# Kernel tuning notes

Measured on AMD Instinct MI355X. Metric: run time of the kernel, lower is better.

Reference implementation:

```python
import jax, jax.numpy as jnp
import numpy as np

EPS = 1e-06


def setup_inputs() -> dict:
    key = jax.random.key(0)
    k1, k2 = jax.random.split(key)
    x = jax.random.normal(k1, (8, 128, 256, 256), dtype=jnp.float32)
    weights = jax.random.normal(k2, (128,), dtype=jnp.float32)
    return {"x": x, "weights": weights}


def reference(x, weights):
    # x: [b, q, h, w]; weights: [q]
    q = weights.shape[0]
    norm_const = jnp.float32(q)
    # use_cumsum=False path: softmax over features, scaled by norm_const
    wt = jax.nn.softmax(weights) * norm_const  # [q]
    # rank[b,i,h,w] = rank of x[b,i,h,w] when sorting dim 1 descending
    order = jnp.argsort(-x, axis=1)            # descending argsort
    rank = jnp.argsort(order, axis=1)          # inverse permutation -> ranks
    # gather per-rank weight and apply 1/sqrt(x^2 + eps)
    return wt[rank] * jax.lax.rsqrt(x * x + jnp.float32(EPS))
```

## Files before the change

kernel.cpp:

```cpp
#include <hip/hip_runtime.h>
#include <math.h>


#define Q    128
#define TCOL 64
#define HW   65536
#define EPSF 1e-6f

__device__ __forceinline__ void acc_ge(int& rk, float a, float b) {
    unsigned long long c, dead;
    asm("v_cmp_ge_f32 %0, %1, %2" : "=s"(c) : "v"(a), "v"(b));
    asm("v_addc_co_u32 %0, %1, %0, 0, %2" : "+v"(rk), "=s"(dead) : "s"(c));
}
__device__ __forceinline__ void acc_gt(int& rk, float a, float b) {
    unsigned long long c, dead;
    asm("v_cmp_gt_f32 %0, %1, %2" : "=s"(c) : "v"(a), "v"(b));
    asm("v_addc_co_u32 %0, %1, %0, 0, %2" : "+v"(rk), "=s"(dead) : "s"(c));
}
__device__ __forceinline__ void pair_upd(int& rkb, int& rka, float va, float vb) {
    unsigned long long c, d1, d2;
    asm("v_cmp_ge_f32 %0, %1, %2" : "=s"(c) : "v"(va), "v"(vb));
    asm("v_addc_co_u32 %0, %1, %0, 0, %2" : "+v"(rkb), "=s"(d1) : "s"(c));
    asm("v_subb_co_u32 %0, %1, %0, 0, %2" : "+v"(rka), "=s"(d2) : "s"(c));
}

__launch_bounds__(256, 4)
__global__ void rank_weight_kernel(const float* __restrict__ x,
                                   const float* __restrict__ weights,
                                   float* __restrict__ out) {
    __shared__ float lds_x[Q][TCOL];
    __shared__ float lds_wt[Q];

    const int tid = threadIdx.x;
    const int g   = blockIdx.x;
    const int b   = g >> 10;
    const int hw0 = (g & 1023) << 6;
    const float* xb = x   + (size_t)b * Q * HW + hw0;
    float*       ob = out + (size_t)b * Q * HW + hw0;

    for (int f = tid; f < Q * (TCOL / 4); f += 256) {
        const int r = f >> 4;
        const int p = f & 15;
        float4 val = *reinterpret_cast<const float4*>(xb + (size_t)r * HW + (p << 2));
        *reinterpret_cast<float4*>(&lds_x[r][p << 2]) = val;
    }

    if (tid < 64) {
        float w0 = weights[tid];
        float w1 = weights[tid + 64];
        float m = fmaxf(w0, w1);
        #pragma unroll
        for (int off = 32; off; off >>= 1) m = fmaxf(m, __shfl_xor(m, off, 64));
        float e0 = __expf(w0 - m), e1 = __expf(w1 - m);
        float s = e0 + e1;
        #pragma unroll
        for (int off = 32; off; off >>= 1) s += __shfl_xor(s, off, 64);
        float scale = 128.0f / s;
        lds_wt[tid]      = e0 * scale;
        lds_wt[tid + 64] = e1 * scale;
    }
    __syncthreads();

    const int wave = tid >> 6;
    const int c    = tid & 63;
    const int R0   = wave * 32;

    float v[32];
    int   rk[32];
    #pragma unroll
    for (int u = 0; u < 32; ++u) v[u] = lds_x[R0 + u][c];
    #pragma unroll
    for (int u = 0; u < 32; ++u) rk[u] = 31 - u;

    #pragma unroll
    for (int a = 0; a < 32; ++a) {
        #pragma unroll
        for (int bq = a + 1; bq < 32; ++bq) pair_upd(rk[bq], rk[a], v[a], v[bq]);
    }

    for (int j = 0; j < R0; j += 2) {
        float w0 = lds_x[j][c];
        float w1 = lds_x[j + 1][c];
        #pragma unroll
        for (int u = 0; u < 32; ++u) acc_ge(rk[u], w0, v[u]);
        #pragma unroll
        for (int u = 0; u < 32; ++u) acc_ge(rk[u], w1, v[u]);
    }
    for (int j = R0 + 32; j < Q; j += 2) {
        float w0 = lds_x[j][c];
        float w1 = lds_x[j + 1][c];
        #pragma unroll
        for (int u = 0; u < 32; ++u) acc_gt(rk[u], w0, v[u]);
        #pragma unroll
        for (int u = 0; u < 32; ++u) acc_gt(rk[u], w1, v[u]);
    }

    #pragma unroll
    for (int u = 0; u < 32; ++u) {
        float wt  = lds_wt[rk[u]];
        float val = v[u];
        ob[(size_t)(R0 + u) * HW + c] = wt * rsqrtf(val * val + EPSF);
    }
}

extern "C" void kernel_launch(void* const* d_in, const int* in_sizes, int n_in,
                              void* d_out, int out_size, void* d_ws, size_t ws_size,
                              hipStream_t stream) {
    const float* x  = (const float*)d_in[0];
    const float* wt = (const float*)d_in[1];
    float* out      = (float*)d_out;

    dim3 grid(8192), block(256);
    hipLaunchKernelGGL(rank_weight_kernel, grid, block, 0, stream, x, wt, out);
}
```

Before: 775.4 us.

## Compare each element pair once using integer keys and packed LDS rank counters

Floats are converted to order-preserving integer keys, and the 128x128 comparison is split so each unordered pair is evaluated exactly once across the four waves. Each wave handles its diagonal triangle plus a balanced share of the cross blocks. Rank contributions go into byte-packed counters accumulated with LDS atomics. The softmax weights stay in registers and are fetched with shuffles instead of an LDS table. This roughly halves the number of comparisons, but each comparison now costs more integer ops, and the change adds LDS atomics and an extra barrier.

```diff
diff --git a/kernel.cpp b/kernel.cpp
--- a/kernel.cpp
+++ b/kernel.cpp
@@ -7,29 +7,16 @@
 #define HW   65536
 #define EPSF 1e-6f
 
-__device__ __forceinline__ void acc_ge(int& rk, float a, float b) {
-    unsigned long long c, dead;
-    asm("v_cmp_ge_f32 %0, %1, %2" : "=s"(c) : "v"(a), "v"(b));
-    asm("v_addc_co_u32 %0, %1, %0, 0, %2" : "+v"(rk), "=s"(dead) : "s"(c));
-}
-__device__ __forceinline__ void acc_gt(int& rk, float a, float b) {
-    unsigned long long c, dead;
-    asm("v_cmp_gt_f32 %0, %1, %2" : "=s"(c) : "v"(a), "v"(b));
-    asm("v_addc_co_u32 %0, %1, %0, 0, %2" : "+v"(rk), "=s"(dead) : "s"(c));
-}
-__device__ __forceinline__ void pair_upd(int& rkb, int& rka, float va, float vb) {
-    unsigned long long c, d1, d2;
-    asm("v_cmp_ge_f32 %0, %1, %2" : "=s"(c) : "v"(va), "v"(vb));
-    asm("v_addc_co_u32 %0, %1, %0, 0, %2" : "+v"(rkb), "=s"(d1) : "s"(c));
-    asm("v_subb_co_u32 %0, %1, %0, 0, %2" : "+v"(rka), "=s"(d2) : "s"(c));
+__device__ __forceinline__ int f2key(int b) {
+    return b ^ (int)(((unsigned)(b >> 31)) >> 1);
 }
 
 __launch_bounds__(256, 4)
 __global__ void rank_weight_kernel(const float* __restrict__ x,
                                    const float* __restrict__ weights,
                                    float* __restrict__ out) {
-    __shared__ float lds_x[Q][TCOL];
-    __shared__ float lds_wt[Q];
+    __shared__ int      lds_k[Q][TCOL];
+    __shared__ unsigned lds_cnt[Q / 4][TCOL];
 
     const int tid = threadIdx.x;
     const int g   = blockIdx.x;
@@ -40,66 +27,125 @@
 
     for (int f = tid; f < Q * (TCOL / 4); f += 256) {
         const int r = f >> 4;
-        const int p = f & 15;
-        float4 val = *reinterpret_cast<const float4*>(xb + (size_t)r * HW + (p << 2));
-        *reinterpret_cast<float4*>(&lds_x[r][p << 2]) = val;
+        const int p = (f & 15) << 2;
+        float4 v = *reinterpret_cast<const float4*>(xb + (size_t)r * HW + p);
+        int4 k;
+        k.x = f2key(__float_as_int(v.x));
+        k.y = f2key(__float_as_int(v.y));
+        k.z = f2key(__float_as_int(v.z));
+        k.w = f2key(__float_as_int(v.w));
+        *reinterpret_cast<int4*>(&lds_k[r][p]) = k;
+    }
+    {
+        uint4 z = {0u, 0u, 0u, 0u};
+        for (int i = tid; i < (Q / 4) * TCOL / 4; i += 256)
+            reinterpret_cast<uint4*>(&lds_cnt[0][0])[i] = z;
     }
 
-    if (tid < 64) {
-        float w0 = weights[tid];
-        float w1 = weights[tid + 64];
-        float m = fmaxf(w0, w1);
+    const int wave = tid >> 6;
+    const int c    = tid & 63;
+
+    float w0s, w1s;
+    {
+        float a0 = weights[c], a1 = weights[c + 64];
+        float m = fmaxf(a0, a1);
         #pragma unroll
         for (int off = 32; off; off >>= 1) m = fmaxf(m, __shfl_xor(m, off, 64));
-        float e0 = __expf(w0 - m), e1 = __expf(w1 - m);
+        float e0 = __expf(a0 - m), e1 = __expf(a1 - m);
         float s = e0 + e1;
         #pragma unroll
         for (int off = 32; off; off >>= 1) s += __shfl_xor(s, off, 64);
-        float scale = 128.0f / s;
-        lds_wt[tid]      = e0 * scale;
-        lds_wt[tid + 64] = e1 * scale;
+        const float scale = 128.0f / s;
+        w0s = e0 * scale;
+        w1s = e1 * scale;
     }
     __syncthreads();
 
-    const int wave = tid >> 6;
-    const int c    = tid & 63;
-    const int R0   = wave * 32;
-
-    float v[32];
-    int   rk[32];
-    #pragma unroll
-    for (int u = 0; u < 32; ++u) v[u] = lds_x[R0 + u][c];
-    #pragma unroll
-    for (int u = 0; u < 32; ++u) rk[u] = 31 - u;
-
-    #pragma unroll
-    for (int a = 0; a < 32; ++a) {
+    {
+        const int B0 = wave << 5;
+        int kD[32], cD[32];
         #pragma unroll
-        for (int bq = a + 1; bq < 32; ++bq) pair_upd(rk[bq], rk[a], v[a], v[bq]);
+        for (int u = 0; u < 32; ++u) kD[u] = lds_k[B0 + u][c];
+        #pragma unroll
+        for (int u = 0; u < 32; ++u) cD[u] = u;
+        #pragma unroll
+        for (int a = 0; a < 32; ++a) {
+            #pragma unroll
+            for (int e = a + 1; e < 32; ++e) {
+                const int t = kD[a] - kD[e];
+                const int s = t >> 31;
+                cD[a] -= s;
+                cD[e] += s;
+            }
+        }
+        #pragma unroll
+        for (int m = 0; m < 8; ++m) {
+            unsigned wv = (unsigned)cD[4 * m]            | ((unsigned)cD[4 * m + 1] << 8)
+                        | ((unsigned)cD[4 * m + 2] << 16) | ((unsigned)cD[4 * m + 3] << 24);
+            atomicAdd(&lds_cnt[(B0 >> 2) + m][c], wv);
+        }
     }
 
-    for (int j = 0; j < R0; j += 2) {
-        float w0 = lds_x[j][c];
-        float w1 = lds_x[j + 1][c];
+    auto cross_job = [&](const int X0, const int XR, const int Y0) {
+        int kY[32], cY[32];
         #pragma unroll
-        for (int u = 0; u < 32; ++u) acc_ge(rk[u], w0, v[u]);
+        for (int u = 0; u < 32; ++u) kY[u] = lds_k[Y0 + u][c];
         #pragma unroll
-        for (int u = 0; u < 32; ++u) acc_ge(rk[u], w1, v[u]);
-    }
-    for (int j = R0 + 32; j < Q; j += 2) {
-        float w0 = lds_x[j][c];
-        float w1 = lds_x[j + 1][c];
+        for (int u = 0; u < 32; ++u) cY[u] = XR;
+        for (int m = 0; m < (XR >> 2); ++m) {
+            const int xr = X0 + (m << 2);
+            int kx0 = lds_k[xr + 0][c];
+            int kx1 = lds_k[xr + 1][c];
+            int kx2 = lds_k[xr + 2][c];
+            int kx3 = lds_k[xr + 3][c];
+            int cx0 = 0, cx1 = 0, cx2 = 0, cx3 = 0;
+            #pragma unroll
+            for (int j = 0; j < 32; ++j) {
+                const int ky = kY[j];
+                const int s0 = (kx0 - ky) >> 31; cx0 -= s0;
+                const int s1 = (kx1 - ky) >> 31; cx1 -= s1;
+                const int s2 = (kx2 - ky) >> 31; cx2 -= s2;
+                const int s3 = (kx3 - ky) >> 31; cx3 -= s3;
+                cY[j] += (s0 + s1) + (s2 + s3);
+            }
+            unsigned wv = (unsigned)cx0         | ((unsigned)cx1 << 8)
+                        | ((unsigned)cx2 << 16) | ((unsigned)cx3 << 24);
+            atomicAdd(&lds_cnt[xr >> 2][c], wv);
+        }
         #pragma unroll
-        for (int u = 0; u < 32; ++u) acc_gt(rk[u], w0, v[u]);
+        for (int n = 0; n < 8; ++n) {
+            unsigned wv = (unsigned)cY[4 * n]            | ((unsigned)cY[4 * n + 1] << 8)
+                        | ((unsigned)cY[4 * n + 2] << 16) | ((unsigned)cY[4 * n + 3] << 24);
+            atomicAdd(&lds_cnt[(Y0 >> 2) + n][c], wv);
+        }
+    };
+
+    const int cXb = (wave == 3) ? 0  : (wave << 5);
+    const int cYb = (wave == 3) ? 96 : ((wave << 5) + 32);
+    cross_job(cXb, 32, cYb);
+
+    const int hXb = wave << 4;
+    const int hYb = (wave < 2) ? 64 : 96;
+    cross_job(hXb, 16, hYb);
+
+    __syncthreads();
+
+    const int R0 = wave << 5;
+    #pragma unroll
+    for (int mw = 0; mw < 8; ++mw) {
+        const unsigned wv = lds_cnt[(R0 >> 2) + mw][c];
         #pragma unroll
-        for (int u = 0; u < 32; ++u) acc_gt(rk[u], w1, v[u]);
-    }
-
-    #pragma unroll
-    for (int u = 0; u < 32; ++u) {
-        float wt  = lds_wt[rk[u]];
-        float val = v[u];
-        ob[(size_t)(R0 + u) * HW + c] = wt * rsqrtf(val * val + EPSF);
+        for (int q = 0; q < 4; ++q) {
+            const int   r    = R0 + (mw << 2) + q;
+            const int   rank = (wv >> (q << 3)) & 0xFF;
+            const int   k    = lds_k[r][c];
+            const float xv   = __int_as_float(f2key(k));
+            const int   rl   = rank & 63;
+            const float wa   = __shfl(w0s, rl, 64);
+            const float wb   = __shfl(w1s, rl, 64);
+            const float wt   = (rank & 64) ? wb : wa;
+            ob[(size_t)r * HW + c] = wt * rsqrtf(xv * xv + EPSF);
+        }
     }
 }
 
```

Measured after the change: 696.1 us. 10.2% less time.
